# Kernel tuning notes

Measured on AMD Instinct MI355X. Metric: run time of the kernel, lower is better.

The kernel has to match this reference:

```python
import jax, jax.numpy as jnp
import numpy as np

GRID_SIZE = 5
SPLINE_ORDER = 3
INPUT_DIM = 4096
BATCH = 4096
N_BASIS = GRID_SIZE + SPLINE_ORDER - 1  # 7


def _extended_knots():
    # Uniform grid on [-1, 1] extended by spline_order knots on each side so the
    # Cox-de Boor recursion is well defined (the original torch code indexes
    # grid[i+k+1] past the end; this is the standard intended knot extension).
    grid = np.linspace(-1.0, 1.0, GRID_SIZE)
    h = grid[1] - grid[0]
    left = grid[0] - h * np.arange(SPLINE_ORDER, 0, -1)
    right = grid[-1] + h * np.arange(1, SPLINE_ORDER + 1)
    return jnp.asarray(np.concatenate([left, grid, right]), dtype=jnp.float32)  # (11,)


def _bspline_basis(x, knots):
    # x: (B, D) -> basis: (B, D, N_BASIS), fully vectorized Cox-de Boor recursion.
    t = knots
    xe = x[..., None]                                   # (B, D, 1)
    Bk = ((xe >= t[:-1]) & (xe < t[1:])).astype(x.dtype)  # degree 0: (B, D, 10)
    for k in range(1, SPLINE_ORDER + 1):
        n = t.shape[0] - k - 1
        left = (xe - t[:n]) / (t[k:k + n] - t[:n]) * Bk[..., :n]
        right = (t[k + 1:k + 1 + n] - xe) / (t[k + 1:k + 1 + n] - t[1:1 + n]) * Bk[..., 1:n + 1]
        Bk = left + right
    return Bk  # (B, D, 7)


def setup_inputs() -> dict:
    key = jax.random.key(0)
    kx, kc = jax.random.split(key)
    x = jax.random.uniform(kx, (BATCH, INPUT_DIM), dtype=jnp.float32, minval=-1.0, maxval=1.0)
    coeffs = jax.random.normal(kc, (INPUT_DIM, N_BASIS), dtype=jnp.float32)
    return {"x": x, "coeffs": coeffs}


def reference(x, coeffs):
    knots = _extended_knots()
    basis = _bspline_basis(x, knots)          # (B, D, K)
    return jnp.einsum('bdk,dk->bd', basis, coeffs)
```

## Files before the change

kernel.cpp:

```cpp
#include <hip/hip_runtime.h>


#define D     4096
#define B     4096
#define NB    7
#define DTILE 256
#define ROWS  16

constexpr int NDT    = D / DTILE;
constexpr int NRT    = B / ROWS;
constexpr int STRIDE = 20;

__global__ __launch_bounds__(256, 8) void
spline_act_kernel(const float* __restrict__ x,
                  const float* __restrict__ coeffs,
                  float* __restrict__ out) {
    __shared__ float sc[DTILE * STRIDE];

    const int bid   = blockIdx.x;
    const int dt    = bid & (NDT - 1);
    const int rowt  = bid >> 4;
    const int dbase = dt * DTILE;

    {
        const int t  = threadIdx.x;
        const int dl = 4 * (t & 63) + (t >> 6);
        const float* crow = coeffs + (size_t)(dbase + dl) * NB;
        float cr[7];
#pragma unroll
        for (int k = 0; k < 7; ++k) cr[k] = crow[k];
        float* bp = &sc[t * STRIDE];
        const float k6 = 1.0f / 6.0f;
#pragma unroll
        for (int c = 0; c < 4; ++c) {
            float A  = cr[c];
            float Bv = cr[c + 1];
            float C  = cr[c + 2];
            float Dv = cr[c + 3];
            float p0 = (A + 4.0f * Bv + C) * k6;
            float p1 = (C - A) * 0.5f;
            float p2 = (A + C) * 0.5f - Bv;
            float p3 = (Dv - A + 3.0f * (Bv - C)) * k6;
            *reinterpret_cast<float4*>(bp + 4 * c) = make_float4(p0, p1, p2, p3);
        }
    }
    __syncthreads();

    const int tid  = threadIdx.x;
    const int pos  = tid & 63;
    const int rsub = tid >> 6;

    const float4* x4 = reinterpret_cast<const float4*>(x);
    float4*       o4 = reinterpret_cast<float4*>(out);

    const int rowbase = rowt * ROWS;

#pragma unroll
    for (int it = 0; it < ROWS / 4; ++it) {
        int row = rowbase + it * 4 + rsub;
        int idx = row * (D / 4) + (dbase >> 2) + pos;

        float4 xv = x4[idx];
        float xs[4] = {xv.x, xv.y, xv.z, xv.w};
        float r[4];

#pragma unroll
        for (int j = 0; j < 4; ++j) {
            float u = (xs[j] + 1.0f) * 2.0f;
            int c = (int)floorf(u);
            c = c < 0 ? 0 : (c > 3 ? 3 : c);
            float s = u - (float)c;

            const float4 cv = *reinterpret_cast<const float4*>(
                &sc[(pos + (j << 6)) * STRIDE + 4 * c]);
            r[j] = fmaf(fmaf(fmaf(cv.w, s, cv.z), s, cv.y), s, cv.x);
        }

        o4[idx] = make_float4(r[0], r[1], r[2], r[3]);
    }
}

extern "C" void kernel_launch(void* const* d_in, const int* in_sizes, int n_in,
                              void* d_out, int out_size, void* d_ws, size_t ws_size,
                              hipStream_t stream) {
    const float* x      = (const float*)d_in[0];
    const float* coeffs = (const float*)d_in[1];
    float* out          = (float*)d_out;

    const int grid = NDT * NRT;
    spline_act_kernel<<<grid, 256, 0, stream>>>(x, coeffs, out);
}
```

Baseline: 112.9 us.

## Enlarge row tile, stage coeffs via LDS, software-pipeline nontemporal x loads

Each block now processes 64 rows instead of 16, which amortizes the per-block coefficient preprocessing over more work and cuts the block count. Coefficients are loaded coalesced as float4 into a raw LDS buffer before the polynomial conversion. The main loop double-buffers four rows of x loads ahead of compute and uses nontemporal loads and stores to avoid cache pollution. The larger tile and extra LDS lower occupancy (launch bounds 4) and reduce the number of blocks available for load balancing.

```diff
diff --git a/kernel.cpp b/kernel.cpp
--- a/kernel.cpp
+++ b/kernel.cpp
@@ -1,82 +1,111 @@
 #include <hip/hip_runtime.h>
 
+
+typedef float f4v __attribute__((ext_vector_type(4)));
 
 #define D     4096
 #define B     4096
 #define NB    7
 #define DTILE 256
-#define ROWS  16
+#define ROWS  64
 
 constexpr int NDT    = D / DTILE;
 constexpr int NRT    = B / ROWS;
 constexpr int STRIDE = 20;
 
-__global__ __launch_bounds__(256, 8) void
+__global__ __launch_bounds__(256, 4) void
 spline_act_kernel(const float* __restrict__ x,
                   const float* __restrict__ coeffs,
                   float* __restrict__ out) {
     __shared__ float sc[DTILE * STRIDE];
+    __shared__ float raw[DTILE * NB];
 
     const int bid   = blockIdx.x;
     const int dt    = bid & (NDT - 1);
     const int rowt  = bid >> 4;
     const int dbase = dt * DTILE;
+    const int t     = threadIdx.x;
 
     {
-        const int t  = threadIdx.x;
+        const f4v* c4 = reinterpret_cast<const f4v*>(coeffs + (size_t)dbase * NB);
+        f4v* r4 = reinterpret_cast<f4v*>(raw);
+        r4[t] = c4[t];
+        if (t < (DTILE * NB / 4) - 256)
+            r4[256 + t] = c4[256 + t];
+        __syncthreads();
+
         const int dl = 4 * (t & 63) + (t >> 6);
-        const float* crow = coeffs + (size_t)(dbase + dl) * NB;
-        float cr[7];
+        float cr[NB];
 #pragma unroll
-        for (int k = 0; k < 7; ++k) cr[k] = crow[k];
+        for (int k = 0; k < NB; ++k) cr[k] = raw[dl * NB + k];
+
+        const float k6 = 1.0f / 6.0f;
         float* bp = &sc[t * STRIDE];
-        const float k6 = 1.0f / 6.0f;
 #pragma unroll
         for (int c = 0; c < 4; ++c) {
             float A  = cr[c];
             float Bv = cr[c + 1];
             float C  = cr[c + 2];
             float Dv = cr[c + 3];
-            float p0 = (A + 4.0f * Bv + C) * k6;
-            float p1 = (C - A) * 0.5f;
-            float p2 = (A + C) * 0.5f - Bv;
-            float p3 = (Dv - A + 3.0f * (Bv - C)) * k6;
-            *reinterpret_cast<float4*>(bp + 4 * c) = make_float4(p0, p1, p2, p3);
+            f4v p;
+            p[0] = (A + 4.0f * Bv + C) * k6;
+            p[1] = (C - A) * 0.5f;
+            p[2] = (A + C) * 0.5f - Bv;
+            p[3] = (Dv - A + 3.0f * (Bv - C)) * k6;
+            *reinterpret_cast<f4v*>(bp + 4 * c) = p;
         }
+        __syncthreads();
     }
-    __syncthreads();
 
-    const int tid  = threadIdx.x;
-    const int pos  = tid & 63;
-    const int rsub = tid >> 6;
+    const int pos  = t & 63;
+    const int rsub = t >> 6;
+    const int lbase = pos * STRIDE;
 
-    const float4* x4 = reinterpret_cast<const float4*>(x);
-    float4*       o4 = reinterpret_cast<float4*>(out);
+    const f4v* x4 = reinterpret_cast<const f4v*>(x);
+    f4v*       o4 = reinterpret_cast<f4v*>(out);
 
-    const int rowbase = rowt * ROWS;
+    const int rstep = 4 * (D / 4);
+    int idx = (rowt * ROWS + rsub) * (D / 4) + (dbase >> 2) + pos;
+
+    auto process = [&](f4v xv, int iidx) {
+        f4v r;
+#pragma unroll
+        for (int j = 0; j < 4; ++j) {
+            float u  = fmaf(xv[j], 2.0f, 2.0f);
+            float cf = floorf(u);
+            cf = fminf(fmaxf(cf, 0.0f), 3.0f);
+            float s  = u - cf;
+            int   c  = (int)cf;
+            const f4v cv = *reinterpret_cast<const f4v*>(
+                &sc[lbase + j * (64 * STRIDE) + (c << 2)]);
+            r[j] = fmaf(fmaf(fmaf(cv[3], s, cv[2]), s, cv[1]), s, cv[0]);
+        }
+        __builtin_nontemporal_store(r, &o4[iidx]);
+    };
+
+    f4v a0 = __builtin_nontemporal_load(&x4[idx + 0 * rstep]);
+    f4v a1 = __builtin_nontemporal_load(&x4[idx + 1 * rstep]);
+    f4v a2 = __builtin_nontemporal_load(&x4[idx + 2 * rstep]);
+    f4v a3 = __builtin_nontemporal_load(&x4[idx + 3 * rstep]);
 
 #pragma unroll
-    for (int it = 0; it < ROWS / 4; ++it) {
-        int row = rowbase + it * 4 + rsub;
-        int idx = row * (D / 4) + (dbase >> 2) + pos;
-
-        float4 xv = x4[idx];
-        float xs[4] = {xv.x, xv.y, xv.z, xv.w};
-        float r[4];
-
-#pragma unroll
-        for (int j = 0; j < 4; ++j) {
-            float u = (xs[j] + 1.0f) * 2.0f;
-            int c = (int)floorf(u);
-            c = c < 0 ? 0 : (c > 3 ? 3 : c);
-            float s = u - (float)c;
-
-            const float4 cv = *reinterpret_cast<const float4*>(
-                &sc[(pos + (j << 6)) * STRIDE + 4 * c]);
-            r[j] = fmaf(fmaf(fmaf(cv.w, s, cv.z), s, cv.y), s, cv.x);
+    for (int g = 0; g < 4; ++g) {
+        f4v b0, b1, b2, b3;
+        const int nidx = idx + 4 * rstep;
+        if (g < 3) {
+            b0 = __builtin_nontemporal_load(&x4[nidx + 0 * rstep]);
+            b1 = __builtin_nontemporal_load(&x4[nidx + 1 * rstep]);
+            b2 = __builtin_nontemporal_load(&x4[nidx + 2 * rstep]);
+            b3 = __builtin_nontemporal_load(&x4[nidx + 3 * rstep]);
+        } else {
+            b0 = a0; b1 = a1; b2 = a2; b3 = a3;
         }
-
-        o4[idx] = make_float4(r[0], r[1], r[2], r[3]);
+        process(a0, idx + 0 * rstep);
+        process(a1, idx + 1 * rstep);
+        process(a2, idx + 2 * rstep);
+        process(a3, idx + 3 * rstep);
+        a0 = b0; a1 = b1; a2 = b2; a3 = b3;
+        idx = nidx;
     }
 }
 
```

New measurement: 119.7 us. 6.0% more time.
